# Optimization experiments

Hardware: AMD Instinct MI355X
Metric: run time of the kernel (lower is better)

Reference implementation:

```python
import jax, jax.numpy as jnp
import numpy as np

# dims: N sentences, L tokens each, M=2 memory slots/sentence, D hidden, H heads
N, L, M, D, H, FF, V, P, LAYERS = 4, 256, 2, 768, 12, 3072, 32000, 1024, 4
DH = D // H


def setup_inputs() -> dict:
    key = jax.random.key(0)
    ks = jax.random.split(key, 20)
    s = 0.02
    inp = {
        'input_ids': jax.random.randint(ks[0], (N, L), 0, V),
        'memory': jax.random.normal(ks[1], (N, M, D), jnp.float32),
        'emb_table': jax.random.normal(ks[2], (V, D), jnp.float32) * s,
        'pos_table': jax.random.normal(ks[3], (P + 2, D), jnp.float32) * s,
        'Wq': jax.random.normal(ks[4], (LAYERS, D, D), jnp.float32) * s,
        'bq': jnp.zeros((LAYERS, D), jnp.float32),
        'Wk': jax.random.normal(ks[5], (LAYERS, D, D), jnp.float32) * s,
        'bk': jnp.zeros((LAYERS, D), jnp.float32),
        'Wv': jax.random.normal(ks[6], (LAYERS, D, D), jnp.float32) * s,
        'bv': jnp.zeros((LAYERS, D), jnp.float32),
        'W1': jax.random.normal(ks[7], (LAYERS, D, FF), jnp.float32) * s,
        'b1': jnp.zeros((LAYERS, FF), jnp.float32),
        'W2': jax.random.normal(ks[8], (LAYERS, FF, D), jnp.float32) * s,
        'b2': jnp.zeros((LAYERS, D), jnp.float32),
        'g1': jnp.ones((LAYERS, D), jnp.float32),
        'be1': jnp.zeros((LAYERS, D), jnp.float32),
        'g2': jnp.ones((LAYERS, D), jnp.float32),
        'be2': jnp.zeros((LAYERS, D), jnp.float32),
    }
    return inp


def _layer_norm(x, g, b):
    mu = jnp.mean(x, axis=-1, keepdims=True)
    var = jnp.mean((x - mu) ** 2, axis=-1, keepdims=True)
    return (x - mu) / jnp.sqrt(var + 1e-5) * g + b


def _encoder(input_ids, memory, emb_table, pos_table, Wq, bq, Wk, bk, Wv, bv,
             W1, b1, W2, b2, g1, be1, g2, be2):
    base = N * M            # token rows start here in the packed input
    T = base + N * L        # total rows (memory rows + token rows)
    Kk = M + L              # keys per query (own memory + own tokens)

    # position embeddings: memory rows get pos (p % M); tokens get id_pos + M
    mem_pos = jnp.tile(jnp.arange(M), N)                    # (N*M,)
    mem = memory.reshape(N * M, D) + pos_table[mem_pos]
    fwd_pos = jnp.tile(jnp.arange(L) + M, N)                # (N*L,)
    tok = emb_table[input_ids.reshape(-1)] + pos_table[fwd_pos]
    x = jnp.concatenate([mem, tok], axis=0)                 # (T, D)

    # per-sentence key set: its M memory rows then its L token rows
    key_pos = jnp.concatenate([
        jnp.arange(N)[:, None] * M + jnp.arange(M)[None, :],
        base + jnp.arange(N)[:, None] * L + jnp.arange(L)[None, :],
    ], axis=1)                                              # (N, Kk)
    sent = jnp.concatenate([jnp.repeat(jnp.arange(N), M),
                            jnp.repeat(jnp.arange(N), L)])  # (T,)
    gidx = key_pos[sent]                                    # (T, Kk)
    # equal-length sentences => the additive mask built by the torch code is
    # all zeros (key_len == max_key_len for every row), so it is omitted.

    scale = 1.0 / np.sqrt(DH)
    for i in range(LAYERS):
        # K/V are linear row-wise, so project once on all rows then gather
        # (identical math to projecting the gathered tgt, without T-fold GEMM)
        q = (x @ Wq[i] + bq[i]).reshape(T, H, DH)
        kf = (x @ Wk[i] + bk[i]).reshape(T, H, DH)
        vf = (x @ Wv[i] + bv[i]).reshape(T, H, DH)
        kg = kf[gidx]                                       # (T, Kk, H, DH)
        vg = vf[gidx]
        scores = jnp.einsum('thd,tkhd->thk', q, kg) * scale
        probs = jax.nn.softmax(scores, axis=-1)
        ctx = jnp.einsum('thk,tkhd->thd', probs, vg).reshape(T, D)
        x = _layer_norm(x + ctx, g1[i], be1[i])
        h = jax.nn.gelu(x @ W1[i] + b1[i], approximate=False)
        x = _layer_norm(x + h @ W2[i] + b2[i], g2[i], be2[i])

    ret = key_pos[:, M:]                                    # (N, L) token rows
    return x[ret]                                           # (N, L, D)


def reference(input_ids, memory, emb_table, pos_table, Wq, bq, Wk, bk, Wv, bv,
              W1, b1, W2, b2, g1, be1, g2, be2):
    return _encoder(input_ids, memory, emb_table, pos_table, Wq, bq, Wk, bk,
                    Wv, bv, W1, b1, W2, b2, g1, be1, g2, be2)
```

## Files before the change

### kernel.cpp

```cpp
#include <hip/hip_runtime.h>
#include <hip/hip_bf16.h>
#include <math.h>

#define N_      4
#define L_      256
#define M_      2
#define D_      768
#define H_      12
#define FF_     3072
#define DH_     64
#define LAYERS_ 4
#define BASE_   8
#define T_      1032
#define TP_     1088
#define KK_     258
#define QS_     2304
#define PS_     264

typedef __bf16 bf16x8 __attribute__((ext_vector_type(8)));
typedef float  f32x4  __attribute__((ext_vector_type(4)));

__device__ __forceinline__ void async_load16(const __hip_bfloat16* g, __hip_bfloat16* l) {
  __builtin_amdgcn_global_load_lds(
      (const __attribute__((address_space(1))) unsigned int*)g,
      (__attribute__((address_space(3))) unsigned int*)l, 16, 0, 0);
}

#define PP_QKV_END_ 6912
#define PP_W1_END_  16128
#define PP_W2_END_  25344
#define PP_B_END_   25380
#define PP_TOTAL_   26412

__global__ __launch_bounds__(256) void preprocess_kernel(
    const float* __restrict__ Wq, const float* __restrict__ Wk,
    const float* __restrict__ Wv, const float* __restrict__ W1,
    const float* __restrict__ W2,
    const float* __restrict__ bq, const float* __restrict__ bk,
    const float* __restrict__ bv,
    const int* __restrict__ ids, const float* __restrict__ memory,
    const float* __restrict__ emb, const float* __restrict__ pos,
    __hip_bfloat16* __restrict__ Wqkvt, __hip_bfloat16* __restrict__ W1t,
    __hip_bfloat16* __restrict__ W2t, float* __restrict__ bqkv,
    float* __restrict__ x, __hip_bfloat16* __restrict__ xb) {
  __shared__ float tile[32][33];
  const int bid = blockIdx.x;
  const int tid = threadIdx.x;

  const float* src;
  __hip_bfloat16* dst;
  int K, N, bx, by;

  if (bid < PP_QKV_END_) {
    int l = bid / 1728, r = bid - l * 1728;
    int which = r / 576; r -= which * 576;
    by = r / 24; bx = r - by * 24;
    src = (which == 0 ? Wq : which == 1 ? Wk : Wv) + (size_t)l * D_ * D_;
    dst = Wqkvt + (size_t)l * QS_ * D_ + (size_t)which * D_ * D_;
    K = D_; N = D_;
  } else if (bid < PP_W1_END_) {
    int r0 = bid - PP_QKV_END_;
    int l = r0 / 2304, r = r0 - l * 2304;
    by = r / 96; bx = r - by * 96;
    src = W1 + (size_t)l * D_ * FF_;
    dst = W1t + (size_t)l * FF_ * D_;
    K = D_; N = FF_;
  } else if (bid < PP_W2_END_) {
    int r0 = bid - PP_W1_END_;
    int l = r0 / 2304, r = r0 - l * 2304;
    by = r / 24; bx = r - by * 24;
    src = W2 + (size_t)l * FF_ * D_;
    dst = W2t + (size_t)l * D_ * FF_;
    K = FF_; N = D_;
  } else if (bid < PP_B_END_) {
    int i = (bid - PP_W2_END_) * 256 + tid;
    int l = i / QS_, j = i - l * QS_;
    float v;
    if (j < D_)            v = bq[l * D_ + j];
    else if (j < 2 * D_)   v = bk[l * D_ + (j - D_)];
    else                   v = bv[l * D_ + (j - 2 * D_)];
    bqkv[i] = v;
    return;
  } else {
    int row = bid - PP_B_END_;
    const float *s2, *p;
    if (row < BASE_) {
      s2 = memory + (long long)row * D_;
      p  = pos + (row & 1) * D_;
    } else {
      int i = row - BASE_;
      int tok = ids[i];
      s2 = emb + (long long)tok * D_;
      p  = pos + (M_ + (i & (L_ - 1))) * D_;
    }
    for (int d = tid; d < D_; d += 256) {
      float v = s2[d] + p[d];
      x[(long long)row * D_ + d]  = v;
      xb[(long long)row * D_ + d] = __float2bfloat16(v);
    }
    return;
  }

  const int k0 = by * 32, n0 = bx * 32;
  const int r = tid >> 5, c = tid & 31;
  #pragma unroll
  for (int i = 0; i < 4; ++i)
    tile[r + i * 8][c] = src[(size_t)(k0 + r + i * 8) * N + n0 + c];
  __syncthreads();
  #pragma unroll
  for (int i = 0; i < 4; ++i)
    dst[(size_t)(n0 + r + i * 8) * K + k0 + c] = __float2bfloat16(tile[c][r + i * 8]);
}

template <int ACT, int WF32, int WBF16, int WVT, int NSPLIT>
__global__ __launch_bounds__(256) void gemm_mfma(
    const __hip_bfloat16* __restrict__ A,
    const __hip_bfloat16* __restrict__ Bt,
    const float* __restrict__ bias,
    float* __restrict__ C,
    __hip_bfloat16* __restrict__ Cb,
    __hip_bfloat16* __restrict__ vt,
    int N, int Ktot) {
  __shared__ __align__(16) __hip_bfloat16 As[2][4][64][32];
  __shared__ __align__(16) __hip_bfloat16 Bs[2][4][64][32];
  const int tid  = threadIdx.x;
  const int lane = tid & 63, wid = tid >> 6;
  const int ln   = lane & 15, qd = lane >> 4;
  const int wm   = wid >> 1, wn = wid & 1;

  const int K = Ktot / NSPLIT;
  const size_t koff = (size_t)blockIdx.z * K;

  const size_t arow = (size_t)(blockIdx.y * 64 + wid * 16 + (lane >> 2)) * Ktot + koff + (lane & 3) * 8;
  const size_t brow = (size_t)(blockIdx.x * 64 + wid * 16 + (lane >> 2)) * Ktot + koff + (lane & 3) * 8;

  f32x4 acc[2][2] = {};

#define STAGE(b, k0) do {                                                     \
    _Pragma("unroll")                                                         \
    for (int s_ = 0; s_ < 4; ++s_) {                                          \
      async_load16(A  + arow + (k0) + s_ * 32, &As[b][s_][wid * 16][0]);      \
      async_load16(Bt + brow + (k0) + s_ * 32, &Bs[b][s_][wid * 16][0]);      \
    }                                                                         \
  } while (0)

  STAGE(0, 0);
  __syncthreads();
  int buf = 0;
  for (int k0 = 0; k0 < K; k0 += 128) {
    if (k0 + 128 < K) STAGE(buf ^ 1, k0 + 128);
    #pragma unroll
    for (int s = 0; s < 4; ++s) {
      bf16x8 a0 = *(const bf16x8*)&As[buf][s][wm * 32 + ln][qd * 8];
      bf16x8 a1 = *(const bf16x8*)&As[buf][s][wm * 32 + 16 + ln][qd * 8];
      bf16x8 b0 = *(const bf16x8*)&Bs[buf][s][wn * 32 + ln][qd * 8];
      bf16x8 b1 = *(const bf16x8*)&Bs[buf][s][wn * 32 + 16 + ln][qd * 8];
      acc[0][0] = __builtin_amdgcn_mfma_f32_16x16x32_bf16(a0, b0, acc[0][0], 0, 0, 0);
      acc[0][1] = __builtin_amdgcn_mfma_f32_16x16x32_bf16(a0, b1, acc[0][1], 0, 0, 0);
      acc[1][0] = __builtin_amdgcn_mfma_f32_16x16x32_bf16(a1, b0, acc[1][0], 0, 0, 0);
      acc[1][1] = __builtin_amdgcn_mfma_f32_16x16x32_bf16(a1, b1, acc[1][1], 0, 0, 0);
    }
    __syncthreads();
    buf ^= 1;
  }
#undef STAGE

  #pragma unroll
  for (int mt = 0; mt < 2; ++mt) {
    #pragma unroll
    for (int nt = 0; nt < 2; ++nt) {
      const int col = blockIdx.x * 64 + wn * 32 + nt * 16 + ln;
      const float bv = (NSPLIT == 1 || blockIdx.z == 0) ? bias[col] : 0.f;
      #pragma unroll
      for (int i = 0; i < 4; ++i) {
        const int row = blockIdx.y * 64 + wm * 32 + mt * 16 + qd * 4 + i;
        float v = acc[mt][nt][i] + bv;
        if (ACT) v = 0.5f * v * (1.f + erff(v * 0.70710678118654752f));
        if (WF32)
          C[(size_t)blockIdx.z * TP_ * N + (size_t)row * N + col] = v;
        if (WVT) {
          if (col < 2 * D_) Cb[(size_t)row * N + col] = __float2bfloat16(v);
          else              vt[(size_t)(col - 2 * D_) * TP_ + row] = __float2bfloat16(v);
        } else if (WBF16) {
          Cb[(size_t)row * N + col] = __float2bfloat16(v);
        }
      }
    }
  }
}

__global__ __launch_bounds__(256) void attn_mfma(
    const __hip_bfloat16* __restrict__ qkv,
    const __hip_bfloat16* __restrict__ vtb,
    float* __restrict__ ctx) {
  __shared__ __align__(16) __hip_bfloat16 Ps[64][PS_];
  const int qt = blockIdx.x, h = blockIdx.y, b = blockIdx.z;
  const int tid = threadIdx.x;
  const int w = tid >> 6, lane = tid & 63, ln = lane & 15, qd = lane >> 4;

  bf16x8 aq0, aq1;
  {
    int j = qt * 64 + w * 16 + ln;
    int tok = (j < 256) ? (BASE_ + b * L_ + j)
            : ((j < KK_) ? (b * M_ + (j - 256)) : (b * M_));
    const __hip_bfloat16* qp = qkv + (size_t)tok * QS_ + h * DH_ + qd * 8;
    aq0 = *(const bf16x8*)qp;
    aq1 = *(const bf16x8*)(qp + 32);
  }

  f32x4 sa[17];
  #pragma unroll
  for (int nt = 0; nt < 17; ++nt) sa[nt] = (f32x4){0.f, 0.f, 0.f, 0.f};
  #pragma unroll
  for (int nt = 0; nt < 17; ++nt) {
    int key = nt * 16 + ln;
    int ktok = (key < 256) ? (BASE_ + b * L_ + key)
             : ((key < KK_) ? (b * M_ + (key - 256)) : (b * M_));
    const __hip_bfloat16* kp = qkv + (size_t)ktok * QS_ + D_ + h * DH_ + qd * 8;
    bf16x8 b0 = *(const bf16x8*)kp;
    bf16x8 b1 = *(const bf16x8*)(kp + 32);
    sa[nt] = __builtin_amdgcn_mfma_f32_16x16x32_bf16(aq0, b0, sa[nt], 0, 0, 0);
    sa[nt] = __builtin_amdgcn_mfma_f32_16x16x32_bf16(aq1, b1, sa[nt], 0, 0, 0);
  }

  #pragma unroll
  for (int i = 0; i < 4; ++i) {
    float v[17];
    #pragma unroll
    for (int nt = 0; nt < 17; ++nt) v[nt] = sa[nt][i] * 0.125f;
    float mx = -1e30f;
    #pragma unroll
    for (int nt = 0; nt < 16; ++nt) mx = fmaxf(mx, v[nt]);
    if (ln < 2) mx = fmaxf(mx, v[16]);
    #pragma unroll
    for (int m = 1; m < 16; m <<= 1) mx = fmaxf(mx, __shfl_xor(mx, m));
    float sum = 0.f;
    #pragma unroll
    for (int nt = 0; nt < 17; ++nt) {
      float e = (nt == 16 && ln >= 2) ? 0.f : __expf(v[nt] - mx);
      v[nt] = e;
      sum += e;
    }
    #pragma unroll
    for (int m = 1; m < 16; m <<= 1) sum += __shfl_xor(sum, m);
    float is = 1.f / sum;
    const int row = w * 16 + qd * 4 + i;
    #pragma unroll
    for (int nt = 0; nt < 17; ++nt)
      if (nt < 16 || ln < 2)
        Ps[row][nt * 16 + ln] = __float2bfloat16(v[nt] * is);
  }

  f32x4 oa[4] = {};
  #pragma unroll
  for (int k0 = 0; k0 < 8; ++k0) {
    bf16x8 ap = *(const bf16x8*)&Ps[w * 16 + ln][k0 * 32 + qd * 8];
    #pragma unroll
    for (int nt = 0; nt < 4; ++nt) {
      const __hip_bfloat16* vp = vtb + (size_t)(h * DH_ + nt * 16 + ln) * TP_
                               + BASE_ + b * L_ + k0 * 32 + qd * 8;
      bf16x8 bv = *(const bf16x8*)vp;
      oa[nt] = __builtin_amdgcn_mfma_f32_16x16x32_bf16(ap, bv, oa[nt], 0, 0, 0);
    }
  }
  {
    float p0[4], p1[4];
    #pragma unroll
    for (int i = 0; i < 4; ++i) {
      p0[i] = __bfloat162float(Ps[w * 16 + qd * 4 + i][256]);
      p1[i] = __bfloat162float(Ps[w * 16 + qd * 4 + i][257]);
    }
    #pragma unroll
    for (int nt = 0; nt < 4; ++nt) {
      const __hip_bfloat16* vp = vtb + (size_t)(h * DH_ + nt * 16 + ln) * TP_ + b * M_;
      float v0 = __bfloat162float(vp[0]);
      float v1 = __bfloat162float(vp[1]);
      #pragma unroll
      for (int i = 0; i < 4; ++i) oa[nt][i] += p0[i] * v0 + p1[i] * v1;
    }
  }

  #pragma unroll
  for (int i = 0; i < 4; ++i) {
    int j = qt * 64 + w * 16 + qd * 4 + i;
    if (j < KK_) {
      int tok = (j < 256) ? (BASE_ + b * L_ + j) : (b * M_ + (j - 256));
      #pragma unroll
      for (int nt = 0; nt < 4; ++nt)
        ctx[(size_t)tok * D_ + h * DH_ + nt * 16 + ln] = oa[nt][i];
    }
  }
}

template <int NS>
__global__ __launch_bounds__(256) void add_ln_kernel(
    float* __restrict__ x, const float* __restrict__ delta,
    const float* __restrict__ g, const float* __restrict__ b,
    __hip_bfloat16* __restrict__ xb, float* __restrict__ out) {
  __shared__ float sred[4];
  __shared__ float sbc;
  const int t = blockIdx.x, tid = threadIdx.x;
  float y[3];
  float s = 0.f;
  #pragma unroll
  for (int i = 0; i < 3; ++i) {
    int d = tid + i * 256;
    float v = x[(long long)t * D_ + d];
    #pragma unroll
    for (int s2 = 0; s2 < NS; ++s2)
      v += delta[(size_t)s2 * TP_ * D_ + (long long)t * D_ + d];
    y[i] = v;
    s += v;
  }
  #pragma unroll
  for (int o = 32; o > 0; o >>= 1) s += __shfl_down(s, o);
  if ((tid & 63) == 0) sred[tid >> 6] = s;
  __syncthreads();
  if (tid == 0) sbc = (sred[0] + sred[1] + sred[2] + sred[3]) * (1.f / D_);
  __syncthreads();
  const float mu = sbc;
  __syncthreads();
  float vs = 0.f;
  #pragma unroll
  for (int i = 0; i < 3; ++i) { float d = y[i] - mu; vs += d * d; }
  #pragma unroll
  for (int o = 32; o > 0; o >>= 1) vs += __shfl_down(vs, o);
  if ((tid & 63) == 0) sred[tid >> 6] = vs;
  __syncthreads();
  if (tid == 0) sbc = (sred[0] + sred[1] + sred[2] + sred[3]) * (1.f / D_);
  __syncthreads();
  const float inv = rsqrtf(sbc + 1e-5f);
  #pragma unroll
  for (int i = 0; i < 3; ++i) {
    int d = tid + i * 256;
    float v = (y[i] - mu) * inv * g[d] + b[d];
    x[(long long)t * D_ + d]  = v;
    xb[(long long)t * D_ + d] = __float2bfloat16(v);
    if (out != nullptr && t >= BASE_)
      out[(size_t)(t - BASE_) * D_ + d] = v;
  }
}

extern "C" void kernel_launch(void* const* d_in, const int* in_sizes, int n_in,
                              void* d_out, int out_size, void* d_ws, size_t ws_size,
                              hipStream_t stream) {
  const int*   ids    = (const int*)  d_in[0];
  const float* memory = (const float*)d_in[1];
  const float* emb    = (const float*)d_in[2];
  const float* pos    = (const float*)d_in[3];
  const float* Wq     = (const float*)d_in[4];
  const float* bq     = (const float*)d_in[5];
  const float* Wk     = (const float*)d_in[6];
  const float* bk     = (const float*)d_in[7];
  const float* Wv     = (const float*)d_in[8];
  const float* bv     = (const float*)d_in[9];
  const float* W1     = (const float*)d_in[10];
  const float* b1     = (const float*)d_in[11];
  const float* W2     = (const float*)d_in[12];
  const float* b2     = (const float*)d_in[13];
  const float* g1     = (const float*)d_in[14];
  const float* be1    = (const float*)d_in[15];
  const float* g2     = (const float*)d_in[16];
  const float* be2    = (const float*)d_in[17];

  char* w = (char*)d_ws;
  float* x    = (float*)w;                      w += (size_t)TP_ * D_ * 4;
  float* cb   = (float*)w;                      w += (size_t)2 * TP_ * D_ * 4;
  float* bqkv = (float*)w;                      w += (size_t)LAYERS_ * QS_ * 4;
  __hip_bfloat16* xb    = (__hip_bfloat16*)w;   w += (size_t)TP_ * D_ * 2;
  __hip_bfloat16* qkvb  = (__hip_bfloat16*)w;   w += (size_t)TP_ * QS_ * 2;
  __hip_bfloat16* vtb   = (__hip_bfloat16*)w;   w += (size_t)D_ * TP_ * 2;
  __hip_bfloat16* hbb   = (__hip_bfloat16*)w;   w += (size_t)TP_ * FF_ * 2;
  __hip_bfloat16* Wqkvt = (__hip_bfloat16*)w;   w += (size_t)LAYERS_ * QS_ * D_ * 2;
  __hip_bfloat16* W1t   = (__hip_bfloat16*)w;   w += (size_t)LAYERS_ * FF_ * D_ * 2;
  __hip_bfloat16* W2t   = (__hip_bfloat16*)w;   w += (size_t)LAYERS_ * D_ * FF_ * 2;

  preprocess_kernel<<<PP_TOTAL_, 256, 0, stream>>>(
      Wq, Wk, Wv, W1, W2, bq, bk, bv, ids, memory, emb, pos,
      Wqkvt, W1t, W2t, bqkv, x, xb);

  for (int i = 0; i < LAYERS_; ++i) {
    gemm_mfma<0, 0, 1, 1, 1><<<dim3(QS_ / 64, TP_ / 64), 256, 0, stream>>>(
        xb, Wqkvt + (size_t)i * QS_ * D_, bqkv + i * QS_, nullptr, qkvb, vtb, QS_, D_);
    attn_mfma<<<dim3(5, H_, N_), 256, 0, stream>>>(qkvb, vtb, cb);
    add_ln_kernel<1><<<T_, 256, 0, stream>>>(x, cb, g1 + i * D_, be1 + i * D_, xb, nullptr);
    gemm_mfma<1, 0, 1, 0, 1><<<dim3(FF_ / 64, TP_ / 64), 256, 0, stream>>>(
        xb, W1t + (size_t)i * FF_ * D_, b1 + i * FF_, nullptr, hbb, nullptr, FF_, D_);
    gemm_mfma<0, 1, 0, 0, 2><<<dim3(D_ / 64, TP_ / 64, 2), 256, 0, stream>>>(
        hbb, W2t + (size_t)i * D_ * FF_, b2 + i * D_, cb, nullptr, nullptr, D_, FF_);
    add_ln_kernel<2><<<T_, 256, 0, stream>>>(
        x, cb, g2 + i * D_, be2 + i * D_, xb,
        (i == LAYERS_ - 1) ? (float*)d_out : nullptr);
  }
}
```

Baseline: 544.5 us.

## Fuse encoder into persistent cooperative megakernel with software grid barriers

Replaces the 25 separate kernel launches with a single persistent cooperative kernel. Blocks loop over work units for each stage (preprocess, QKV GEMM, attention, LN, FFN GEMMs) and separate the stages with a custom atomic grid barrier. The aim is to remove launch overhead and inter-kernel gaps. In exchange, grid-stride loops cap parallelism at the resident block count, and each barrier costs spin-waiting plus a serialized poll by block 0. A fallback multi-kernel path runs if the cooperative launch fails.

```diff
diff --git a/kernel.cpp b/kernel.cpp
--- a/kernel.cpp
+++ b/kernel.cpp
@@ -20,33 +20,71 @@
 typedef __bf16 bf16x8 __attribute__((ext_vector_type(8)));
 typedef float  f32x4  __attribute__((ext_vector_type(4)));
 
-__device__ __forceinline__ void async_load16(const __hip_bfloat16* g, __hip_bfloat16* l) {
-  __builtin_amdgcn_global_load_lds(
-      (const __attribute__((address_space(1))) unsigned int*)g,
-      (__attribute__((address_space(3))) unsigned int*)l, 16, 0, 0);
-}
-
 #define PP_QKV_END_ 6912
 #define PP_W1_END_  16128
 #define PP_W2_END_  25344
 #define PP_B_END_   25380
 #define PP_TOTAL_   26412
 
-__global__ __launch_bounds__(256) void preprocess_kernel(
-    const float* __restrict__ Wq, const float* __restrict__ Wk,
-    const float* __restrict__ Wv, const float* __restrict__ W1,
-    const float* __restrict__ W2,
-    const float* __restrict__ bq, const float* __restrict__ bk,
-    const float* __restrict__ bv,
-    const int* __restrict__ ids, const float* __restrict__ memory,
-    const float* __restrict__ emb, const float* __restrict__ pos,
-    __hip_bfloat16* __restrict__ Wqkvt, __hip_bfloat16* __restrict__ W1t,
-    __hip_bfloat16* __restrict__ W2t, float* __restrict__ bqkv,
-    float* __restrict__ x, __hip_bfloat16* __restrict__ xb) {
-  __shared__ float tile[32][33];
-  const int bid = blockIdx.x;
+struct __align__(16) SharedU {
+  union {
+    struct { __hip_bfloat16 As[2][4][64][32]; __hip_bfloat16 Bs[2][4][64][32]; } g;
+    __hip_bfloat16 Ps[64][PS_];
+    float tile[32][33];
+  } u;
+  float sred[4];
+  float sbc;
+};
+
+struct KP {
+  const int* ids; const float* memory; const float* emb; const float* pos;
+  const float* Wq; const float* bq; const float* Wk; const float* bk;
+  const float* Wv; const float* bv; const float* W1; const float* b1;
+  const float* W2; const float* b2; const float* g1; const float* be1;
+  const float* g2; const float* be2;
+  float *x, *cb, *bqkv;
+  __hip_bfloat16 *xb, *qkvb, *vtb, *hbb, *Wqkvt, *W1t, *W2t;
+  float* out;
+  unsigned* bar;
+  unsigned nblk;
+};
+
+__device__ __forceinline__ void async_load16(const __hip_bfloat16* g, __hip_bfloat16* l) {
+  __builtin_amdgcn_global_load_lds(
+      (const __attribute__((address_space(1))) unsigned int*)g,
+      (__attribute__((address_space(3))) unsigned int*)l, 16, 0, 0);
+}
+
+__device__ __forceinline__ void gbar(const KP& p, unsigned& idx) {
+  __syncthreads();
+  __threadfence();
+  if (threadIdx.x == 0) {
+    const unsigned tgt = idx + 1;
+    __hip_atomic_fetch_add(p.bar + (blockIdx.x & 63) * 16, 1u,
+                           __ATOMIC_RELAXED, __HIP_MEMORY_SCOPE_AGENT);
+    unsigned* rel = p.bar + 64 * 16;
+    if (blockIdx.x == 0) {
+      unsigned sum;
+      do {
+        sum = 0;
+        #pragma unroll
+        for (int i = 0; i < 64; ++i)
+          sum += __hip_atomic_load(p.bar + i * 16, __ATOMIC_RELAXED,
+                                   __HIP_MEMORY_SCOPE_AGENT);
+      } while (sum < tgt * p.nblk);
+      __hip_atomic_store(rel, tgt, __ATOMIC_RELAXED, __HIP_MEMORY_SCOPE_AGENT);
+    } else {
+      while (__hip_atomic_load(rel, __ATOMIC_RELAXED, __HIP_MEMORY_SCOPE_AGENT) < tgt)
+        __builtin_amdgcn_s_sleep(1);
+    }
+  }
+  __syncthreads();
+  __threadfence();
+  idx++;
+}
+
+__device__ __forceinline__ void pp_unit(int bid, const KP& p, SharedU& sh) {
   const int tid = threadIdx.x;
-
   const float* src;
   __hip_bfloat16* dst;
   int K, N, bx, by;
@@ -55,48 +93,48 @@
     int l = bid / 1728, r = bid - l * 1728;
     int which = r / 576; r -= which * 576;
     by = r / 24; bx = r - by * 24;
-    src = (which == 0 ? Wq : which == 1 ? Wk : Wv) + (size_t)l * D_ * D_;
-    dst = Wqkvt + (size_t)l * QS_ * D_ + (size_t)which * D_ * D_;
+    src = (which == 0 ? p.Wq : which == 1 ? p.Wk : p.Wv) + (size_t)l * D_ * D_;
+    dst = p.Wqkvt + (size_t)l * QS_ * D_ + (size_t)which * D_ * D_;
     K = D_; N = D_;
   } else if (bid < PP_W1_END_) {
     int r0 = bid - PP_QKV_END_;
     int l = r0 / 2304, r = r0 - l * 2304;
     by = r / 96; bx = r - by * 96;
-    src = W1 + (size_t)l * D_ * FF_;
-    dst = W1t + (size_t)l * FF_ * D_;
+    src = p.W1 + (size_t)l * D_ * FF_;
+    dst = p.W1t + (size_t)l * FF_ * D_;
     K = D_; N = FF_;
   } else if (bid < PP_W2_END_) {
     int r0 = bid - PP_W1_END_;
     int l = r0 / 2304, r = r0 - l * 2304;
     by = r / 24; bx = r - by * 24;
-    src = W2 + (size_t)l * FF_ * D_;
-    dst = W2t + (size_t)l * D_ * FF_;
+    src = p.W2 + (size_t)l * FF_ * D_;
+    dst = p.W2t + (size_t)l * D_ * FF_;
     K = FF_; N = D_;
   } else if (bid < PP_B_END_) {
     int i = (bid - PP_W2_END_) * 256 + tid;
     int l = i / QS_, j = i - l * QS_;
     float v;
-    if (j < D_)            v = bq[l * D_ + j];
-    else if (j < 2 * D_)   v = bk[l * D_ + (j - D_)];
-    else                   v = bv[l * D_ + (j - 2 * D_)];
-    bqkv[i] = v;
+    if (j < D_)            v = p.bq[l * D_ + j];
+    else if (j < 2 * D_)   v = p.bk[l * D_ + (j - D_)];
+    else                   v = p.bv[l * D_ + (j - 2 * D_)];
+    p.bqkv[i] = v;
     return;
   } else {
     int row = bid - PP_B_END_;
-    const float *s2, *p;
+    const float *s2, *pp;
     if (row < BASE_) {
-      s2 = memory + (long long)row * D_;
-      p  = pos + (row & 1) * D_;
+      s2 = p.memory + (long long)row * D_;
+      pp = p.pos + (row & 1) * D_;
     } else {
       int i = row - BASE_;
-      int tok = ids[i];
-      s2 = emb + (long long)tok * D_;
-      p  = pos + (M_ + (i & (L_ - 1))) * D_;
+      int tok = p.ids[i];
+      s2 = p.emb + (long long)tok * D_;
+      pp = p.pos + (M_ + (i & (L_ - 1))) * D_;
     }
     for (int d = tid; d < D_; d += 256) {
-      float v = s2[d] + p[d];
-      x[(long long)row * D_ + d]  = v;
-      xb[(long long)row * D_ + d] = __float2bfloat16(v);
+      float v = s2[d] + pp[d];
+      p.x[(long long)row * D_ + d]  = v;
+      p.xb[(long long)row * D_ + d] = __float2bfloat16(v);
     }
     return;
   }
@@ -105,56 +143,53 @@
   const int r = tid >> 5, c = tid & 31;
   #pragma unroll
   for (int i = 0; i < 4; ++i)
-    tile[r + i * 8][c] = src[(size_t)(k0 + r + i * 8) * N + n0 + c];
+    sh.u.tile[r + i * 8][c] = src[(size_t)(k0 + r + i * 8) * N + n0 + c];
   __syncthreads();
   #pragma unroll
   for (int i = 0; i < 4; ++i)
-    dst[(size_t)(n0 + r + i * 8) * K + k0 + c] = __float2bfloat16(tile[c][r + i * 8]);
+    dst[(size_t)(n0 + r + i * 8) * K + k0 + c] = __float2bfloat16(sh.u.tile[c][r + i * 8]);
+  __syncthreads();
 }
 
 template <int ACT, int WF32, int WBF16, int WVT, int NSPLIT>
-__global__ __launch_bounds__(256) void gemm_mfma(
-    const __hip_bfloat16* __restrict__ A,
-    const __hip_bfloat16* __restrict__ Bt,
-    const float* __restrict__ bias,
-    float* __restrict__ C,
-    __hip_bfloat16* __restrict__ Cb,
-    __hip_bfloat16* __restrict__ vt,
-    int N, int Ktot) {
-  __shared__ __align__(16) __hip_bfloat16 As[2][4][64][32];
-  __shared__ __align__(16) __hip_bfloat16 Bs[2][4][64][32];
+__device__ __forceinline__ void gemm_tile(
+    int bx, int by, int bz,
+    const __hip_bfloat16* __restrict__ A, const __hip_bfloat16* __restrict__ Bt,
+    const float* __restrict__ bias, float* __restrict__ C,
+    __hip_bfloat16* __restrict__ Cb, __hip_bfloat16* __restrict__ vt,
+    int N, int Ktot, SharedU& sh) {
   const int tid  = threadIdx.x;
   const int lane = tid & 63, wid = tid >> 6;
   const int ln   = lane & 15, qd = lane >> 4;
   const int wm   = wid >> 1, wn = wid & 1;
 
   const int K = Ktot / NSPLIT;
-  const size_t koff = (size_t)blockIdx.z * K;
-
-  const size_t arow = (size_t)(blockIdx.y * 64 + wid * 16 + (lane >> 2)) * Ktot + koff + (lane & 3) * 8;
-  const size_t brow = (size_t)(blockIdx.x * 64 + wid * 16 + (lane >> 2)) * Ktot + koff + (lane & 3) * 8;
+  const size_t koff = (size_t)bz * K;
+  const size_t arow = (size_t)(by * 64 + wid * 16 + (lane >> 2)) * Ktot + koff + (lane & 3) * 8;
+  const size_t brow = (size_t)(bx * 64 + wid * 16 + (lane >> 2)) * Ktot + koff + (lane & 3) * 8;
 
   f32x4 acc[2][2] = {};
 
-#define STAGE(b, k0) do {                                                     \
-    _Pragma("unroll")                                                         \
-    for (int s_ = 0; s_ < 4; ++s_) {                                          \
-      async_load16(A  + arow + (k0) + s_ * 32, &As[b][s_][wid * 16][0]);      \
-      async_load16(Bt + brow + (k0) + s_ * 32, &Bs[b][s_][wid * 16][0]);      \
-    }                                                                         \
+#define STAGE_(b, k0)                                                          \
+  do {                                                                         \
+    _Pragma("unroll")                                                          \
+    for (int s_ = 0; s_ < 4; ++s_) {                                           \
+      async_load16(A  + arow + (k0) + s_ * 32, &sh.u.g.As[b][s_][wid * 16][0]);\
+      async_load16(Bt + brow + (k0) + s_ * 32, &sh.u.g.Bs[b][s_][wid * 16][0]);\
+    }                                                                          \
   } while (0)
 
-  STAGE(0, 0);
+  STAGE_(0, 0);
   __syncthreads();
   int buf = 0;
   for (int k0 = 0; k0 < K; k0 += 128) {
-    if (k0 + 128 < K) STAGE(buf ^ 1, k0 + 128);
+    if (k0 + 128 < K) STAGE_(buf ^ 1, k0 + 128);
     #pragma unroll
     for (int s = 0; s < 4; ++s) {
-      bf16x8 a0 = *(const bf16x8*)&As[buf][s][wm * 32 + ln][qd * 8];
-      bf16x8 a1 = *(const bf16x8*)&As[buf][s][wm * 32 + 16 + ln][qd * 8];
-      bf16x8 b0 = *(const bf16x8*)&Bs[buf][s][wn * 32 + ln][qd * 8];
-      bf16x8 b1 = *(const bf16x8*)&Bs[buf][s][wn * 32 + 16 + ln][qd * 8];
+      bf16x8 a0 = *(const bf16x8*)&sh.u.g.As[buf][s][wm * 32 + ln][qd * 8];
+      bf16x8 a1 = *(const bf16x8*)&sh.u.g.As[buf][s][wm * 32 + 16 + ln][qd * 8];
+      bf16x8 b0 = *(const bf16x8*)&sh.u.g.Bs[buf][s][wn * 32 + ln][qd * 8];
+      bf16x8 b1 = *(const bf16x8*)&sh.u.g.Bs[buf][s][wn * 32 + 16 + ln][qd * 8];
       acc[0][0] = __builtin_amdgcn_mfma_f32_16x16x32_bf16(a0, b0, acc[0][0], 0, 0, 0);
       acc[0][1] = __builtin_amdgcn_mfma_f32_16x16x32_bf16(a0, b1, acc[0][1], 0, 0, 0);
       acc[1][0] = __builtin_amdgcn_mfma_f32_16x16x32_bf16(a1, b0, acc[1][0], 0, 0, 0);
@@ -163,21 +198,21 @@
     __syncthreads();
     buf ^= 1;
   }
-#undef STAGE
+#undef STAGE_
 
   #pragma unroll
   for (int mt = 0; mt < 2; ++mt) {
     #pragma unroll
     for (int nt = 0; nt < 2; ++nt) {
-      const int col = blockIdx.x * 64 + wn * 32 + nt * 16 + ln;
-      const float bv = (NSPLIT == 1 || blockIdx.z == 0) ? bias[col] : 0.f;
+      const int col = bx * 64 + wn * 32 + nt * 16 + ln;
+      const float bv = (NSPLIT == 1 || bz == 0) ? bias[col] : 0.f;
       #pragma unroll
       for (int i = 0; i < 4; ++i) {
-        const int row = blockIdx.y * 64 + wm * 32 + mt * 16 + qd * 4 + i;
+        const int row = by * 64 + wm * 32 + mt * 16 + qd * 4 + i;
         float v = acc[mt][nt][i] + bv;
         if (ACT) v = 0.5f * v * (1.f + erff(v * 0.70710678118654752f));
         if (WF32)
-          C[(size_t)blockIdx.z * TP_ * N + (size_t)row * N + col] = v;
+          C[(size_t)bz * TP_ * N + (size_t)row * N + col] = v;
         if (WVT) {
           if (col < 2 * D_) Cb[(size_t)row * N + col] = __float2bfloat16(v);
           else              vt[(size_t)(col - 2 * D_) * TP_ + row] = __float2bfloat16(v);
@@ -189,12 +224,10 @@
   }
 }
 
-__global__ __launch_bounds__(256) void attn_mfma(
-    const __hip_bfloat16* __restrict__ qkv,
-    const __hip_bfloat16* __restrict__ vtb,
-    float* __restrict__ ctx) {
-  __shared__ __align__(16) __hip_bfloat16 Ps[64][PS_];
-  const int qt = blockIdx.x, h = blockIdx.y, b = blockIdx.z;
+__device__ __forceinline__ void attn_unit(int qt, int h, int b, const KP& p, SharedU& sh) {
+  const __hip_bfloat16* qkv = p.qkvb;
+  const __hip_bfloat16* vtb = p.vtb;
+  float* ctx = p.cb;
   const int tid = threadIdx.x;
   const int w = tid >> 6, lane = tid & 63, ln = lane & 15, qd = lane >> 4;
 
@@ -248,13 +281,13 @@
     #pragma unroll
     for (int nt = 0; nt < 17; ++nt)
       if (nt < 16 || ln < 2)
-        Ps[row][nt * 16 + ln] = __float2bfloat16(v[nt] * is);
+        sh.u.Ps[row][nt * 16 + ln] = __float2bfloat16(v[nt] * is);
   }
 
   f32x4 oa[4] = {};
   #pragma unroll
   for (int k0 = 0; k0 < 8; ++k0) {
-    bf16x8 ap = *(const bf16x8*)&Ps[w * 16 + ln][k0 * 32 + qd * 8];
+    bf16x8 ap = *(const bf16x8*)&sh.u.Ps[w * 16 + ln][k0 * 32 + qd * 8];
     #pragma unroll
     for (int nt = 0; nt < 4; ++nt) {
       const __hip_bfloat16* vp = vtb + (size_t)(h * DH_ + nt * 16 + ln) * TP_
@@ -267,8 +300,8 @@
     float p0[4], p1[4];
     #pragma unroll
     for (int i = 0; i < 4; ++i) {
-      p0[i] = __bfloat162float(Ps[w * 16 + qd * 4 + i][256]);
-      p1[i] = __bfloat162float(Ps[w * 16 + qd * 4 + i][257]);
+      p0[i] = __bfloat162float(sh.u.Ps[w * 16 + qd * 4 + i][256]);
+      p1[i] = __bfloat162float(sh.u.Ps[w * 16 + qd * 4 + i][257]);
     }
     #pragma unroll
     for (int nt = 0; nt < 4; ++nt) {
@@ -293,103 +326,194 @@
 }
 
 template <int NS>
-__global__ __launch_bounds__(256) void add_ln_kernel(
-    float* __restrict__ x, const float* __restrict__ delta,
-    const float* __restrict__ g, const float* __restrict__ b,
-    __hip_bfloat16* __restrict__ xb, float* __restrict__ out) {
-  __shared__ float sred[4];
-  __shared__ float sbc;
-  const int t = blockIdx.x, tid = threadIdx.x;
+__device__ __forceinline__ void ln_row(
+    int t, const KP& p, const float* __restrict__ g, const float* __restrict__ b,
+    float* __restrict__ out, SharedU& sh) {
+  const int tid = threadIdx.x;
   float y[3];
   float s = 0.f;
   #pragma unroll
   for (int i = 0; i < 3; ++i) {
     int d = tid + i * 256;
-    float v = x[(long long)t * D_ + d];
+    float v = p.x[(long long)t * D_ + d];
     #pragma unroll
     for (int s2 = 0; s2 < NS; ++s2)
-      v += delta[(size_t)s2 * TP_ * D_ + (long long)t * D_ + d];
+      v += p.cb[(size_t)s2 * TP_ * D_ + (long long)t * D_ + d];
     y[i] = v;
     s += v;
   }
   #pragma unroll
   for (int o = 32; o > 0; o >>= 1) s += __shfl_down(s, o);
-  if ((tid & 63) == 0) sred[tid >> 6] = s;
-  __syncthreads();
-  if (tid == 0) sbc = (sred[0] + sred[1] + sred[2] + sred[3]) * (1.f / D_);
-  __syncthreads();
-  const float mu = sbc;
+  if ((tid & 63) == 0) sh.sred[tid >> 6] = s;
+  __syncthreads();
+  if (tid == 0) sh.sbc = (sh.sred[0] + sh.sred[1] + sh.sred[2] + sh.sred[3]) * (1.f / D_);
+  __syncthreads();
+  const float mu = sh.sbc;
   __syncthreads();
   float vs = 0.f;
   #pragma unroll
   for (int i = 0; i < 3; ++i) { float d = y[i] - mu; vs += d * d; }
   #pragma unroll
   for (int o = 32; o > 0; o >>= 1) vs += __shfl_down(vs, o);
-  if ((tid & 63) == 0) sred[tid >> 6] = vs;
-  __syncthreads();
-  if (tid == 0) sbc = (sred[0] + sred[1] + sred[2] + sred[3]) * (1.f / D_);
-  __syncthreads();
-  const float inv = rsqrtf(sbc + 1e-5f);
+  if ((tid & 63) == 0) sh.sred[tid >> 6] = vs;
+  __syncthreads();
+  if (tid == 0) sh.sbc = (sh.sred[0] + sh.sred[1] + sh.sred[2] + sh.sred[3]) * (1.f / D_);
+  __syncthreads();
+  const float inv = rsqrtf(sh.sbc + 1e-5f);
   #pragma unroll
   for (int i = 0; i < 3; ++i) {
     int d = tid + i * 256;
     float v = (y[i] - mu) * inv * g[d] + b[d];
-    x[(long long)t * D_ + d]  = v;
-    xb[(long long)t * D_ + d] = __float2bfloat16(v);
+    p.x[(long long)t * D_ + d]  = v;
+    p.xb[(long long)t * D_ + d] = __float2bfloat16(v);
     if (out != nullptr && t >= BASE_)
       out[(size_t)(t - BASE_) * D_ + d] = v;
   }
+}
+
+__global__ __launch_bounds__(256, 2) void encoder_mega(KP p) {
+  __shared__ SharedU sh;
+  unsigned bidx = 0;
+  const unsigned nb = p.nblk;
+
+  for (unsigned u = blockIdx.x; u < PP_TOTAL_; u += nb) pp_unit((int)u, p, sh);
+  gbar(p, bidx);
+
+  for (int l = 0; l < LAYERS_; ++l) {
+    const __hip_bfloat16* Wt = p.Wqkvt + (size_t)l * QS_ * D_;
+    for (unsigned u = blockIdx.x; u < 36u * 17u; u += nb)
+      gemm_tile<0, 0, 1, 1, 1>((int)(u % 36u), (int)(u / 36u), 0,
+                               p.xb, Wt, p.bqkv + l * QS_, nullptr, p.qkvb, p.vtb,
+                               QS_, D_, sh);
+    gbar(p, bidx);
+
+    for (unsigned u = blockIdx.x; u < 240u; u += nb)
+      attn_unit((int)(u % 5u), (int)((u / 5u) % 12u), (int)(u / 60u), p, sh);
+    gbar(p, bidx);
+
+    for (unsigned u = blockIdx.x; u < (unsigned)T_; u += nb)
+      ln_row<1>((int)u, p, p.g1 + l * D_, p.be1 + l * D_, nullptr, sh);
+    gbar(p, bidx);
+
+    for (unsigned u = blockIdx.x; u < 48u * 17u; u += nb)
+      gemm_tile<1, 0, 1, 0, 1>((int)(u % 48u), (int)(u / 48u), 0,
+                               p.xb, p.W1t + (size_t)l * FF_ * D_, p.b1 + l * FF_,
+                               nullptr, p.hbb, nullptr, FF_, D_, sh);
+    gbar(p, bidx);
+
+    for (unsigned u = blockIdx.x; u < 2u * 204u; u += nb) {
+      unsigned z = u / 204u, r = u % 204u;
+      gemm_tile<0, 1, 0, 0, 2>((int)(r % 12u), (int)(r / 12u), (int)z,
+                               p.hbb, p.W2t + (size_t)l * D_ * FF_, p.b2 + l * D_,
+                               p.cb, nullptr, nullptr, D_, FF_, sh);
+    }
+    gbar(p, bidx);
+
+    for (unsigned u = blockIdx.x; u < (unsigned)T_; u += nb)
+      ln_row<2>((int)u, p, p.g2 + l * D_, p.be2 + l * D_,
+                (l == LAYERS_ - 1) ? p.out : nullptr, sh);
+    if (l != LAYERS_ - 1) gbar(p, bidx);
+  }
+}
+
+__global__ __launch_bounds__(256) void pp_k(KP p) {
+  __shared__ SharedU sh;
+  pp_unit((int)blockIdx.x, p, sh);
+}
+__global__ __launch_bounds__(256) void gemm_qkv_k(KP p, int l) {
+  __shared__ SharedU sh;
+  gemm_tile<0, 0, 1, 1, 1>(blockIdx.x, blockIdx.y, 0, p.xb,
+                           p.Wqkvt + (size_t)l * QS_ * D_, p.bqkv + l * QS_,
+                           nullptr, p.qkvb, p.vtb, QS_, D_, sh);
+}
+__global__ __launch_bounds__(256) void gemm_ffn1_k(KP p, int l) {
+  __shared__ SharedU sh;
+  gemm_tile<1, 0, 1, 0, 1>(blockIdx.x, blockIdx.y, 0, p.xb,
+                           p.W1t + (size_t)l * FF_ * D_, p.b1 + l * FF_,
+                           nullptr, p.hbb, nullptr, FF_, D_, sh);
+}
+__global__ __launch_bounds__(256) void gemm_ffn2_k(KP p, int l) {
+  __shared__ SharedU sh;
+  gemm_tile<0, 1, 0, 0, 2>(blockIdx.x, blockIdx.y, blockIdx.z, p.hbb,
+                           p.W2t + (size_t)l * D_ * FF_, p.b2 + l * D_,
+                           p.cb, nullptr, nullptr, D_, FF_, sh);
+}
+__global__ __launch_bounds__(256) void attn_k(KP p) {
+  __shared__ SharedU sh;
+  attn_unit(blockIdx.x, blockIdx.y, blockIdx.z, p, sh);
+}
+__global__ __launch_bounds__(256) void ln1_k(KP p, int l) {
+  __shared__ SharedU sh;
+  ln_row<1>((int)blockIdx.x, p, p.g1 + l * D_, p.be1 + l * D_, nullptr, sh);
+}
+__global__ __launch_bounds__(256) void ln2_k(KP p, int l) {
+  __shared__ SharedU sh;
+  ln_row<2>((int)blockIdx.x, p, p.g2 + l * D_, p.be2 + l * D_,
+            (l == LAYERS_ - 1) ? p.out : nullptr, sh);
 }
 
 extern "C" void kernel_launch(void* const* d_in, const int* in_sizes, int n_in,
                               void* d_out, int out_size, void* d_ws, size_t ws_size,
                               hipStream_t stream) {
-  const int*   ids    = (const int*)  d_in[0];
-  const float* memory = (const float*)d_in[1];
-  const float* emb    = (const float*)d_in[2];
-  const float* pos    = (const float*)d_in[3];
-  const float* Wq     = (const float*)d_in[4];
-  const float* bq     = (const float*)d_in[5];
-  const float* Wk     = (const float*)d_in[6];
-  const float* bk     = (const float*)d_in[7];
-  const float* Wv     = (const float*)d_in[8];
-  const float* bv     = (const float*)d_in[9];
-  const float* W1     = (const float*)d_in[10];
-  const float* b1     = (const float*)d_in[11];
-  const float* W2     = (const float*)d_in[12];
-  const float* b2     = (const float*)d_in[13];
-  const float* g1     = (const float*)d_in[14];
-  const float* be1    = (const float*)d_in[15];
-  const float* g2     = (const float*)d_in[16];
-  const float* be2    = (const float*)d_in[17];
+  KP p;
+  p.ids    = (const int*)  d_in[0];
+  p.memory = (const float*)d_in[1];
+  p.emb    = (const float*)d_in[2];
+  p.pos    = (const float*)d_in[3];
+  p.Wq     = (const float*)d_in[4];
+  p.bq     = (const float*)d_in[5];
+  p.Wk     = (const float*)d_in[6];
+  p.bk     = (const float*)d_in[7];
+  p.Wv     = (const float*)d_in[8];
+  p.bv     = (const float*)d_in[9];
+  p.W1     = (const float*)d_in[10];
+  p.b1     = (const float*)d_in[11];
+  p.W2     = (const float*)d_in[12];
+  p.b2     = (const float*)d_in[13];
+  p.g1     = (const float*)d_in[14];
+  p.be1    = (const float*)d_in[15];
+  p.g2     = (const float*)d_in[16];
+  p.be2    = (const float*)d_in[17];
+  p.out    = (float*)d_out;
 
   char* w = (char*)d_ws;
-  float* x    = (float*)w;                      w += (size_t)TP_ * D_ * 4;
-  float* cb   = (float*)w;                      w += (size_t)2 * TP_ * D_ * 4;
-  float* bqkv = (float*)w;                      w += (size_t)LAYERS_ * QS_ * 4;
-  __hip_bfloat16* xb    = (__hip_bfloat16*)w;   w += (size_t)TP_ * D_ * 2;
-  __hip_bfloat16* qkvb  = (__hip_bfloat16*)w;   w += (size_t)TP_ * QS_ * 2;
-  __hip_bfloat16* vtb   = (__hip_bfloat16*)w;   w += (size_t)D_ * TP_ * 2;
-  __hip_bfloat16* hbb   = (__hip_bfloat16*)w;   w += (size_t)TP_ * FF_ * 2;
-  __hip_bfloat16* Wqkvt = (__hip_bfloat16*)w;   w += (size_t)LAYERS_ * QS_ * D_ * 2;
-  __hip_bfloat16* W1t   = (__hip_bfloat16*)w;   w += (size_t)LAYERS_ * FF_ * D_ * 2;
-  __hip_bfloat16* W2t   = (__hip_bfloat16*)w;   w += (size_t)LAYERS_ * D_ * FF_ * 2;
-
-  preprocess_kernel<<<PP_TOTAL_, 256, 0, stream>>>(
-      Wq, Wk, Wv, W1, W2, bq, bk, bv, ids, memory, emb, pos,
-      Wqkvt, W1t, W2t, bqkv, x, xb);
-
-  for (int i = 0; i < LAYERS_; ++i) {
-    gemm_mfma<0, 0, 1, 1, 1><<<dim3(QS_ / 64, TP_ / 64), 256, 0, stream>>>(
-        xb, Wqkvt + (size_t)i * QS_ * D_, bqkv + i * QS_, nullptr, qkvb, vtb, QS_, D_);
-    attn_mfma<<<dim3(5, H_, N_), 256, 0, stream>>>(qkvb, vtb, cb);
-    add_ln_kernel<1><<<T_, 256, 0, stream>>>(x, cb, g1 + i * D_, be1 + i * D_, xb, nullptr);
-    gemm_mfma<1, 0, 1, 0, 1><<<dim3(FF_ / 64, TP_ / 64), 256, 0, stream>>>(
-        xb, W1t + (size_t)i * FF_ * D_, b1 + i * FF_, nullptr, hbb, nullptr, FF_, D_);
-    gemm_mfma<0, 1, 0, 0, 2><<<dim3(D_ / 64, TP_ / 64, 2), 256, 0, stream>>>(
-        hbb, W2t + (size_t)i * D_ * FF_, b2 + i * D_, cb, nullptr, nullptr, D_, FF_);
-    add_ln_kernel<2><<<T_, 256, 0, stream>>>(
-        x, cb, g2 + i * D_, be2 + i * D_, xb,
-        (i == LAYERS_ - 1) ? (float*)d_out : nullptr);
-  }
-}
+  p.bar   = (unsigned*)w;                  w += 8192;
+  p.x     = (float*)w;                     w += (size_t)TP_ * D_ * 4;
+  p.cb    = (float*)w;                     w += (size_t)2 * TP_ * D_ * 4;
+  p.bqkv  = (float*)w;                     w += (size_t)LAYERS_ * QS_ * 4;
+  p.xb    = (__hip_bfloat16*)w;            w += (size_t)TP_ * D_ * 2;
+  p.qkvb  = (__hip_bfloat16*)w;            w += (size_t)TP_ * QS_ * 2;
+  p.vtb   = (__hip_bfloat16*)w;            w += (size_t)D_ * TP_ * 2;
+  p.hbb   = (__hip_bfloat16*)w;            w += (size_t)TP_ * FF_ * 2;
+  p.Wqkvt = (__hip_bfloat16*)w;            w += (size_t)LAYERS_ * QS_ * D_ * 2;
+  p.W1t   = (__hip_bfloat16*)w;            w += (size_t)LAYERS_ * FF_ * D_ * 2;
+  p.W2t   = (__hip_bfloat16*)w;            w += (size_t)LAYERS_ * D_ * FF_ * 2;
+
+  static int nbs = 0;
+  if (nbs == 0) {
+    int nb = 0;
+    if (hipOccupancyMaxActiveBlocksPerMultiprocessor(
+            &nb, (const void*)encoder_mega, 256, 0) != hipSuccess || nb < 1)
+      nb = 1;
+    if (nb > 4) nb = 4;
+    nbs = nb * 256;
+  }
+  p.nblk = (unsigned)nbs;
+
+  hipMemsetAsync(p.bar, 0, 8192, stream);
+  void* args[] = { &p };
+  hipError_t err = hipLaunchCooperativeKernel(
+      (const void*)encoder_mega, dim3((unsigned)nbs), dim3(256), args, 0, stream);
+
+  if (err != hipSuccess) {
+    pp_k<<<PP_TOTAL_, 256, 0, stream>>>(p);
+    for (int i = 0; i < LAYERS_; ++i) {
+      gemm_qkv_k<<<dim3(QS_ / 64, TP_ / 64), 256, 0, stream>>>(p, i);
+      attn_k<<<dim3(5, H_, N_), 256, 0, stream>>>(p);
+      ln1_k<<<T_, 256, 0, stream>>>(p, i);
+      gemm_ffn1_k<<<dim3(FF_ / 64, TP_ / 64), 256, 0, stream>>>(p, i);
+      gemm_ffn2_k<<<dim3(D_ / 64, TP_ / 64, 2), 256, 0, stream>>>(p, i);
+      ln2_k<<<T_, 256, 0, stream>>>(p, i);
+    }
+  }
+}
```

Measured after the change: 1.929 ms. 254% more time.
